# Kernel tuning notes

Measured on AMD Instinct MI355X. Metric: run time of the kernel, lower is better.

Reference implementation:

```python
import jax, jax.numpy as jnp
import numpy as np

N = 50000
E = 800000
IN_C = 512
HID = 256
NUM_CLASS = (10, 25, 16, 350)


def _glorot(key, shape):
    fan_in, fan_out = shape[0], shape[1]
    lim = float(np.sqrt(6.0 / (fan_in + fan_out)))
    return jax.random.uniform(key, shape, jnp.float32, -lim, lim)


def setup_inputs() -> dict:
    key = jax.random.key(0)
    ks = jax.random.split(key, 16)
    x = jax.random.normal(ks[0], (N, IN_C), jnp.float32)
    edge_index = jax.random.randint(ks[1], (2, E), 0, N, jnp.int32)
    inp = {"x": x, "edge_index": edge_index}
    # gc1
    inp["W1"] = _glorot(ks[2], (IN_C, HID)); inp["b1"] = jnp.zeros((HID,), jnp.float32)
    # four GCNConv heads
    names = ["type", "school", "time", "author"]
    for i, (nm, nc) in enumerate(zip(names, NUM_CLASS)):
        inp[f"Wg_{nm}"] = _glorot(ks[3 + i], (HID, nc))
        inp[f"bg_{nm}"] = jnp.zeros((nc,), jnp.float32)
        inp[f"Wc_{nm}"] = _glorot(ks[7 + i], (nc, nc))
        inp[f"bc_{nm}"] = jnp.zeros((nc,), jnp.float32)
    return inp


def gcn_conv(x, W, b, src, dst, n):
    # GCNConv: out = D^{-1/2} (A + I) D^{-1/2} (x W) + b, symmetric norm.
    xw = x @ W  # [N, out]
    ones = jnp.ones((src.shape[0],), xw.dtype)
    deg = jax.ops.segment_sum(ones, dst, num_segments=n) + 1.0  # +1 from self-loop
    dinv = jax.lax.rsqrt(deg)
    norm = dinv[src] * dinv[dst]  # [E]
    agg = jax.ops.segment_sum(xw[src] * norm[:, None], dst, num_segments=n)
    # self-loop contribution: norm_ii = dinv_i^2
    return agg + xw * (dinv * dinv)[:, None] + b


def reference(x, edge_index, W1, b1,
              Wg_type, bg_type, Wc_type, bc_type,
              Wg_school, bg_school, Wc_school, bc_school,
              Wg_time, bg_time, Wc_time, bc_time,
              Wg_author, bg_author, Wc_author, bc_author):
    src, dst = edge_index[0], edge_index[1]
    n = x.shape[0]
    h = jax.nn.relu(gcn_conv(x, W1, b1, src, dst, n))  # dropout is identity in eval

    def head(Wg, bg, Wc, bc):
        g = gcn_conv(h, Wg, bg, src, dst, n)
        return jax.nn.softmax(g @ Wc + bc, axis=-1)

    out_type = head(Wg_type, bg_type, Wc_type, bc_type)
    out_school = head(Wg_school, bg_school, Wc_school, bc_school)
    out_time = head(Wg_time, bg_time, Wc_time, bc_time)
    out_author = head(Wg_author, bg_author, Wc_author, bc_author)
    return (out_type, out_school, out_time, out_author)
```

## Files before the change

kernel.cpp:

```cpp
#include <hip/hip_runtime.h>
#include <hip/hip_bf16.h>
#include <cstdint>
#include <cstddef>
#include <math.h>

#define NN 50000
#define NE 800000
#define INC 512
#define HIDC 256
#define NBLK ((NN + 255) / 256)

typedef __attribute__((ext_vector_type(8))) short s8v;
typedef __attribute__((ext_vector_type(4))) float f4v;
typedef unsigned int u32;

__device__ __forceinline__ float b2f(unsigned short u) {
    return __uint_as_float(((unsigned)u) << 16);
}
__device__ __forceinline__ unsigned short f2b(float f) {
    __hip_bfloat16 h = __float2bfloat16(f);
    return *reinterpret_cast<unsigned short*>(&h);
}
__device__ __forceinline__ void gload16(const void* g, void* l) {
    __builtin_amdgcn_global_load_lds(
        (const __attribute__((address_space(1))) u32*)g,
        (__attribute__((address_space(3))) u32*)l, 16, 0, 0);
}

__global__ void k_deg_count(const int* __restrict__ dst, int* __restrict__ cnt, int e) {
    int i = blockIdx.x * 256 + threadIdx.x;
    if (i < e) atomicAdd(&cnt[dst[i]], 1);
}
__global__ void k_scan1(const int* __restrict__ cnt, int* __restrict__ excl,
                        int* __restrict__ bsum, float* __restrict__ dinv, int n) {
    __shared__ int s[256];
    int i = blockIdx.x * 256 + threadIdx.x;
    int v = (i < n) ? cnt[i] : 0;
    if (i < n) dinv[i] = rsqrtf((float)v + 1.0f);
    s[threadIdx.x] = v;
    __syncthreads();
    for (int off = 1; off < 256; off <<= 1) {
        int t = (threadIdx.x >= off) ? s[threadIdx.x - off] : 0;
        __syncthreads();
        s[threadIdx.x] += t;
        __syncthreads();
    }
    if (i < n) excl[i] = s[threadIdx.x] - v;
    if (threadIdx.x == 255) bsum[blockIdx.x] = s[255];
}
__global__ void k_scan2(int* __restrict__ bsum, int* __restrict__ bsumx, int nb) {
    __shared__ int s[256];
    int t = threadIdx.x;
    int v = (t < nb) ? bsum[t] : 0;
    s[t] = v;
    __syncthreads();
    for (int off = 1; off < 256; off <<= 1) {
        int tt = (t >= off) ? s[t - off] : 0;
        __syncthreads();
        s[t] += tt;
        __syncthreads();
    }
    if (t < nb) bsumx[t] = s[t] - v;
}
__global__ void k_scan3(int* __restrict__ rowptr, const int* __restrict__ bsumx, int n, int e) {
    int i = blockIdx.x * 256 + threadIdx.x;
    if (i < n) rowptr[i] += bsumx[blockIdx.x];
    if (i == 0) rowptr[n] = e;
}
__global__ void k_fill(const int* __restrict__ src, const int* __restrict__ dst,
                       const int* __restrict__ rowptr, int* __restrict__ cursor,
                       int* __restrict__ col, int e) {
    int i = blockIdx.x * 256 + threadIdx.x;
    if (i >= e) return;
    int d = dst[i];
    int pos = rowptr[d] + atomicAdd(&cursor[d], 1);
    col[pos] = src[i];
}

__global__ void k_tr2(const float* __restrict__ Wg3, const float* __restrict__ Wc3,
                      float* __restrict__ Wg3t, float* __restrict__ Wc3t) {
    int t = blockIdx.x * 256 + threadIdx.x;
    if (t < 256 * 350) { int k = t / 350, i = t - k * 350; Wg3t[i * 256 + k] = Wg3[t]; }
    if (t < 350 * 350) { int i = t / 350, j = t - i * 350; Wc3t[j * 350 + i] = Wc3[t]; }
}

__global__ void k_prep(const float* __restrict__ W1,
                       const float* __restrict__ Wg0, const float* __restrict__ Wc0,
                       const float* __restrict__ bg0, const float* __restrict__ bc0,
                       const float* __restrict__ Wg1, const float* __restrict__ Wc1,
                       const float* __restrict__ bg1, const float* __restrict__ bc1,
                       const float* __restrict__ Wg2, const float* __restrict__ Wc2,
                       const float* __restrict__ bg2, const float* __restrict__ bc2,
                       const float* __restrict__ Wg3, const float* __restrict__ Wc3,
                       const float* __restrict__ bg3, const float* __restrict__ bc3,
                       const float* __restrict__ Wg3t, const float* __restrict__ Wc3t,
                       unsigned short* __restrict__ W1t_sw, unsigned short* __restrict__ Wft_sw,
                       float* __restrict__ bfv)
{
    __shared__ float Wcj[352];
    int b = blockIdx.x, tid = threadIdx.x;
    if (b < 512) {
        int t = b * 256 + tid;
        int c = t >> 9, k = t & 511;
        int chs = ((k >> 3) & 7) ^ (c & 7);
        W1t_sw[(size_t)(k >> 6) * 16384 + c * 64 + chs * 8 + (k & 7)] = f2b(W1[(size_t)k * 256 + c]);
    } else if (b < 960) {
        int j = b - 512, k = tid;
        float s = 0.f;
        if (j < 350) {
            for (int i = tid; i < 350; i += 256) Wcj[i] = Wc3t[(size_t)j * 350 + i];
            __syncthreads();
            for (int i = 0; i < 350; ++i) s += Wg3t[i * 256 + k] * Wcj[i];
        } else if (j >= 352 && j < 362) {
            int jj = j - 352; for (int i = 0; i < 10; ++i) s += Wg0[k * 10 + i] * Wc0[i * 10 + jj];
        } else if (j >= 362 && j < 387) {
            int jj = j - 362; for (int i = 0; i < 25; ++i) s += Wg1[k * 25 + i] * Wc1[i * 25 + jj];
        } else if (j >= 387 && j < 403) {
            int jj = j - 387; for (int i = 0; i < 16; ++i) s += Wg2[k * 16 + i] * Wc2[i * 16 + jj];
        }
        int chs = ((k >> 3) & 7) ^ (j & 7);
        Wft_sw[(size_t)(k >> 6) * 28672 + j * 64 + chs * 8 + (k & 7)] = f2b(s);
    } else {
        int j = (b - 960) * 256 + tid;
        if (j >= 448) return;
        float s = 0.f;
        if (j < 350)                  { s = bc3[j]; for (int i = 0; i < 350; ++i) s += bg3[i] * Wc3[(size_t)i * 350 + j]; }
        else if (j >= 352 && j < 362) { int jj = j - 352; s = bc0[jj]; for (int i = 0; i < 10; ++i) s += bg0[i] * Wc0[i * 10 + jj]; }
        else if (j >= 362 && j < 387) { int jj = j - 362; s = bc1[jj]; for (int i = 0; i < 25; ++i) s += bg1[i] * Wc1[i * 25 + jj]; }
        else if (j >= 387 && j < 403) { int jj = j - 387; s = bc2[jj]; for (int i = 0; i < 16; ++i) s += bg2[i] * Wc2[i * 16 + jj]; }
        bfv[j] = s;
    }
}

__global__ __launch_bounds__(256, 4) void gemm1_conv(
    const float* __restrict__ X, const unsigned short* __restrict__ Bsw,
    unsigned short* __restrict__ C, int M)
{
    __shared__ s8v lds[512 + 2048];
    const int t = threadIdx.x;
    const int lane = t & 63, wv = t >> 6;
    const int wvM = wv >> 1, wvN = wv & 1;
    const int l15 = lane & 15, lq = lane >> 4;
    const int row0 = blockIdx.x * 64;

    const int arow = t >> 2;
    int gr = row0 + arow; if (gr >= M) gr = M - 1;
    const float* asrc = X + (size_t)gr * INC + (t & 3) * 16;
    const int ach0 = (t & 3) * 2;
    s8v* aw0 = &lds[arow * 8 + (ach0 ^ (arow & 7))];
    s8v* aw1 = &lds[arow * 8 + ((ach0 + 1) ^ (arow & 7))];

    f4v acc[2][8] = {};
    for (int kb = 0; kb < 8; ++kb) {
        float4 f0 = *(const float4*)(asrc + kb * 64);
        float4 f1 = *(const float4*)(asrc + kb * 64 + 4);
        float4 f2 = *(const float4*)(asrc + kb * 64 + 8);
        float4 f3 = *(const float4*)(asrc + kb * 64 + 12);
        s8v o0, o1;
        o0[0]=(short)f2b(f0.x); o0[1]=(short)f2b(f0.y); o0[2]=(short)f2b(f0.z); o0[3]=(short)f2b(f0.w);
        o0[4]=(short)f2b(f1.x); o0[5]=(short)f2b(f1.y); o0[6]=(short)f2b(f1.z); o0[7]=(short)f2b(f1.w);
        o1[0]=(short)f2b(f2.x); o1[1]=(short)f2b(f2.y); o1[2]=(short)f2b(f2.z); o1[3]=(short)f2b(f2.w);
        o1[4]=(short)f2b(f3.x); o1[5]=(short)f2b(f3.y); o1[6]=(short)f2b(f3.z); o1[7]=(short)f2b(f3.w);
        *aw0 = o0; *aw1 = o1;
#pragma unroll
        for (int sB = 0; sB < 8; ++sB) {
            int ci = (wv * 8 + sB) * 64 + lane;
            gload16(Bsw + ((size_t)kb * 2048 + ci) * 8, (void*)&lds[512 + (wv * 8 + sB) * 64]);
        }
        __syncthreads();
#pragma unroll
        for (int kk = 0; kk < 2; ++kk) {
            const int chr = (kk * 4 + lq) ^ (l15 & 7);
            s8v a0 = lds[(wvM * 32 + l15) * 8 + chr];
            s8v a1 = lds[(wvM * 32 + 16 + l15) * 8 + chr];
#pragma unroll
            for (int cf = 0; cf < 8; ++cf) {
                s8v bf = lds[512 + (wvN * 128 + cf * 16 + l15) * 8 + chr];
                acc[0][cf] = __builtin_amdgcn_mfma_f32_16x16x32_bf16(a0, bf, acc[0][cf], 0, 0, 0);
                acc[1][cf] = __builtin_amdgcn_mfma_f32_16x16x32_bf16(a1, bf, acc[1][cf], 0, 0, 0);
            }
        }
        __syncthreads();
    }
#pragma unroll
    for (int rf = 0; rf < 2; ++rf)
#pragma unroll
    for (int r = 0; r < 4; ++r) {
        int row = row0 + wvM * 32 + rf * 16 + lq * 4 + r;
        if (row >= M) continue;
#pragma unroll
        for (int cf = 0; cf < 8; ++cf)
            C[(size_t)row * HIDC + wvN * 128 + cf * 16 + l15] = f2b(acc[rf][cf][r]);
    }
}

template <bool RELU, bool BIAS, bool SWZ>
__global__ __launch_bounds__(256) void k_gather2(
    const unsigned short* __restrict__ feat, const int* __restrict__ rowptr,
    const int* __restrict__ col, const float* __restrict__ dinv,
    const float* __restrict__ bias, unsigned short* __restrict__ out, int n)
{
    int unit = (blockIdx.x * 256 + threadIdx.x) >> 5;
    int l32 = threadIdx.x & 31;
    if (unit >= n) return;
    float di = dinv[unit];
    int p0 = rowptr[unit], p1 = rowptr[unit + 1];
    int deg = p1 - p0;
    int myc = 0; float mydj = 0.f;
    if (l32 < deg) { myc = col[p0 + l32]; mydj = dinv[myc]; }
    float acc[8] = {};
    int dmin = deg < 32 ? deg : 32;
    int base = threadIdx.x & 32;
#pragma unroll 2
    for (int q = 0; q < dmin; ++q) {
        int j = __shfl(myc, base + q);
        float dj = __shfl(mydj, base + q);
        s8v v = *(const s8v*)(feat + (size_t)j * HIDC + l32 * 8);
#pragma unroll
        for (int c = 0; c < 8; ++c) acc[c] += dj * b2f((unsigned short)v[c]);
    }
    for (int p = p0 + 32; p < p1; ++p) {
        int j = col[p];
        float dj = dinv[j];
        s8v v = *(const s8v*)(feat + (size_t)j * HIDC + l32 * 8);
#pragma unroll
        for (int c = 0; c < 8; ++c) acc[c] += dj * b2f((unsigned short)v[c]);
    }
    s8v sv = *(const s8v*)(feat + (size_t)unit * HIDC + l32 * 8);
    float dd = di * di;
    s8v o;
#pragma unroll
    for (int c = 0; c < 8; ++c) {
        float r = di * acc[c] + dd * b2f((unsigned short)sv[c]);
        if (BIAS) r += bias[l32 * 8 + c];
        if (RELU) r = fmaxf(r, 0.f);
        o[c] = (short)f2b(r);
    }
    int outch = SWZ ? ((l32 & 24) | ((l32 & 7) ^ (unit & 7))) : l32;
    *(s8v*)(out + (size_t)unit * HIDC + outch * 8) = o;
}

__global__ __launch_bounds__(512, 4) void gemm2_heads(
    const unsigned short* __restrict__ Asw, const unsigned short* __restrict__ Bsw,
    const float* __restrict__ bfv,
    float* __restrict__ o0, float* __restrict__ o1,
    float* __restrict__ o2, float* __restrict__ o3, int M)
{
    __shared__ s8v lds[512 + 3584];
    const int t = threadIdx.x;
    const int lane = t & 63, wv = t >> 6;
    const int wvM = wv >> 2, wvN = wv & 3;
    const int l15 = lane & 15, lq = lane >> 4;
    const int row0 = blockIdx.x * 64;

    f4v acc[2][7] = {};
    for (int kb = 0; kb < 4; ++kb) {
        {
            int ci = wv * 64 + lane;
            int arow = ci >> 3, ch = ci & 7;
            int grow = row0 + arow; if (grow >= M) grow = M - 1;
            gload16(Asw + (size_t)grow * HIDC + (kb * 8 + ch) * 8, (void*)&lds[wv * 64]);
        }
#pragma unroll
        for (int sB = 0; sB < 7; ++sB) {
            int ci = (wv * 7 + sB) * 64 + lane;
            gload16(Bsw + ((size_t)kb * 3584 + ci) * 8, (void*)&lds[512 + (wv * 7 + sB) * 64]);
        }
        __syncthreads();
#pragma unroll
        for (int kk = 0; kk < 2; ++kk) {
            const int chr = (kk * 4 + lq) ^ (l15 & 7);
            s8v a0 = lds[(wvM * 32 + l15) * 8 + chr];
            s8v a1 = lds[(wvM * 32 + 16 + l15) * 8 + chr];
#pragma unroll
            for (int cf = 0; cf < 7; ++cf) {
                s8v bf = lds[512 + (wvN * 112 + cf * 16 + l15) * 8 + chr];
                acc[0][cf] = __builtin_amdgcn_mfma_f32_16x16x32_bf16(a0, bf, acc[0][cf], 0, 0, 0);
                acc[1][cf] = __builtin_amdgcn_mfma_f32_16x16x32_bf16(a1, bf, acc[1][cf], 0, 0, 0);
            }
        }
        __syncthreads();
    }
    float* smx = (float*)lds;
#pragma unroll
    for (int cf = 0; cf < 7; ++cf) {
        float bb = bfv[wvN * 112 + cf * 16 + l15];
#pragma unroll
        for (int rf = 0; rf < 2; ++rf)
#pragma unroll
        for (int r = 0; r < 4; ++r) acc[rf][cf][r] += bb;
    }
#pragma unroll
    for (int rf = 0; rf < 2; ++rf)
#pragma unroll
    for (int r = 0; r < 4; ++r) {
        float ma = -1e30f, m1 = -1e30f, m2 = -1e30f, m3 = -1e30f;
#pragma unroll
        for (int cf = 0; cf < 7; ++cf) {
            int colc = wvN * 112 + cf * 16 + l15;
            float v = acc[rf][cf][r];
            if (colc < 350) ma = fmaxf(ma, v);
            else if (colc >= 352 && colc < 362) m1 = fmaxf(m1, v);
            else if (colc >= 362 && colc < 387) m2 = fmaxf(m2, v);
            else if (colc >= 387 && colc < 403) m3 = fmaxf(m3, v);
        }
#pragma unroll
        for (int o = 8; o; o >>= 1) {
            ma = fmaxf(ma, __shfl_xor(ma, o));
            m1 = fmaxf(m1, __shfl_xor(m1, o));
            m2 = fmaxf(m2, __shfl_xor(m2, o));
            m3 = fmaxf(m3, __shfl_xor(m3, o));
        }
        int rowl = wvM * 32 + rf * 16 + lq * 4 + r;
        if (l15 == 0) {
            smx[rowl * 4 + wvN] = ma;
            if (wvN == 3) {
                smx[512 + rowl * 3 + 0] = m1;
                smx[512 + rowl * 3 + 1] = m2;
                smx[512 + rowl * 3 + 2] = m3;
            }
        }
    }
    __syncthreads();
#pragma unroll
    for (int rf = 0; rf < 2; ++rf)
#pragma unroll
    for (int r = 0; r < 4; ++r) {
        int rowl = wvM * 32 + rf * 16 + lq * 4 + r;
        float am = fmaxf(fmaxf(smx[rowl * 4 + 0], smx[rowl * 4 + 1]),
                         fmaxf(smx[rowl * 4 + 2], smx[rowl * 4 + 3]));
        float m1 = 0.f, m2 = 0.f, m3 = 0.f;
        if (wvN == 3) {
            m1 = smx[512 + rowl * 3 + 0];
            m2 = smx[512 + rowl * 3 + 1];
            m3 = smx[512 + rowl * 3 + 2];
        }
        float sa = 0.f, s1 = 0.f, s2 = 0.f, s3 = 0.f;
#pragma unroll
        for (int cf = 0; cf < 7; ++cf) {
            int colc = wvN * 112 + cf * 16 + l15;
            float v = acc[rf][cf][r];
            float e = 0.f;
            if (colc < 350)                     { e = __expf(v - am); sa += e; }
            else if (colc >= 352 && colc < 362) { e = __expf(v - m1); s1 += e; }
            else if (colc >= 362 && colc < 387) { e = __expf(v - m2); s2 += e; }
            else if (colc >= 387 && colc < 403) { e = __expf(v - m3); s3 += e; }
            acc[rf][cf][r] = e;
        }
#pragma unroll
        for (int o = 8; o; o >>= 1) {
            sa += __shfl_xor(sa, o); s1 += __shfl_xor(s1, o);
            s2 += __shfl_xor(s2, o); s3 += __shfl_xor(s3, o);
        }
        if (l15 == 0) {
            smx[256 + rowl * 4 + wvN] = sa;
            if (wvN == 3) {
                smx[704 + rowl * 3 + 0] = s1;
                smx[704 + rowl * 3 + 1] = s2;
                smx[704 + rowl * 3 + 2] = s3;
            }
        }
    }
    __syncthreads();
#pragma unroll
    for (int rf = 0; rf < 2; ++rf)
#pragma unroll
    for (int r = 0; r < 4; ++r) {
        int rowl = wvM * 32 + rf * 16 + lq * 4 + r;
        int row = row0 + rowl;
        if (row >= M) continue;
        float ia = 1.f / (smx[256 + rowl * 4 + 0] + smx[256 + rowl * 4 + 1] +
                          smx[256 + rowl * 4 + 2] + smx[256 + rowl * 4 + 3]);
        float i1 = 0.f, i2 = 0.f, i3 = 0.f;
        if (wvN == 3) {
            i1 = 1.f / smx[704 + rowl * 3 + 0];
            i2 = 1.f / smx[704 + rowl * 3 + 1];
            i3 = 1.f / smx[704 + rowl * 3 + 2];
        }
#pragma unroll
        for (int cf = 0; cf < 7; ++cf) {
            int colc = wvN * 112 + cf * 16 + l15;
            float e = acc[rf][cf][r];
            if (colc < 350)                     o3[(size_t)row * 350 + colc]        = e * ia;
            else if (colc >= 352 && colc < 362) o0[(size_t)row * 10 + (colc - 352)] = e * i1;
            else if (colc >= 362 && colc < 387) o1[(size_t)row * 25 + (colc - 362)] = e * i2;
            else if (colc >= 387 && colc < 403) o2[(size_t)row * 16 + (colc - 387)] = e * i3;
        }
    }
}

extern "C" void kernel_launch(void* const* d_in, const int* in_sizes, int n_in,
                              void* d_out, int out_size, void* d_ws, size_t ws_size,
                              hipStream_t stream)
{
    const float* x   = (const float*)d_in[0];
    const int*   ei  = (const int*)d_in[1];
    const float* W1  = (const float*)d_in[2];
    const float* b1  = (const float*)d_in[3];
    const float* Wg0 = (const float*)d_in[4];
    const float* bg0 = (const float*)d_in[5];
    const float* Wc0 = (const float*)d_in[6];
    const float* bc0 = (const float*)d_in[7];
    const float* Wg1 = (const float*)d_in[8];
    const float* bg1 = (const float*)d_in[9];
    const float* Wc1 = (const float*)d_in[10];
    const float* bc1 = (const float*)d_in[11];
    const float* Wg2 = (const float*)d_in[12];
    const float* bg2 = (const float*)d_in[13];
    const float* Wc2 = (const float*)d_in[14];
    const float* bc2 = (const float*)d_in[15];
    const float* Wg3 = (const float*)d_in[16];
    const float* bg3 = (const float*)d_in[17];
    const float* Wc3 = (const float*)d_in[18];
    const float* bc3 = (const float*)d_in[19];
    const int* srcI = ei;
    const int* dstI = ei + NE;

    char* ws = (char*)d_ws;
    size_t off = 0;
    auto alloc = [&](size_t bytes) { void* p = ws + off; off += (bytes + 255) & ~(size_t)255; return p; };
    float* dinv   = (float*)alloc(50176 * 4);
    int*   rowptr = (int*)  alloc(50432 * 4);
    int*   cnt    = (int*)  alloc(2 * 50176 * 4);
    int*   cursor = cnt + 50176;
    int*   bsum   = (int*)  alloc(1024);
    int*   bsumx  = (int*)  alloc(1024);
    int*   col    = (int*)  alloc((size_t)NE * 4);
    unsigned short* W1t_sw = (unsigned short*)alloc(256 * 512 * 2);
    unsigned short* Wft_sw = (unsigned short*)alloc(448 * 256 * 2);
    float* bfv   = (float*)alloc(448 * 4);
    float* Wg3t  = (float*)alloc(350 * 256 * 4);
    float* Wc3t  = (float*)alloc(350 * 350 * 4);
    unsigned short* xwb = (unsigned short*)alloc((size_t)NN * HIDC * 2);
    unsigned short* hb  = (unsigned short*)alloc((size_t)NN * HIDC * 2);
    unsigned short* ahb = xwb;

    float* out0 = (float*)d_out;
    float* out1 = out0 + (size_t)NN * 10;
    float* out2 = out1 + (size_t)NN * 25;
    float* out3 = out2 + (size_t)NN * 16;

    hipMemsetAsync(cnt, 0, 2 * 50176 * 4, stream);
    k_deg_count<<<(NE + 255) / 256, 256, 0, stream>>>(dstI, cnt, NE);
    k_scan1<<<NBLK, 256, 0, stream>>>(cnt, rowptr, bsum, dinv, NN);
    k_scan2<<<1, 256, 0, stream>>>(bsum, bsumx, NBLK);
    k_scan3<<<NBLK, 256, 0, stream>>>(rowptr, bsumx, NN, NE);
    k_fill<<<(NE + 255) / 256, 256, 0, stream>>>(srcI, dstI, rowptr, cursor, col, NE);

    k_tr2<<<(350 * 350 + 255) / 256, 256, 0, stream>>>(Wg3, Wc3, Wg3t, Wc3t);
    k_prep<<<962, 256, 0, stream>>>(W1,
                                    Wg0, Wc0, bg0, bc0, Wg1, Wc1, bg1, bc1,
                                    Wg2, Wc2, bg2, bc2, Wg3, Wc3, bg3, bc3,
                                    Wg3t, Wc3t, W1t_sw, Wft_sw, bfv);

    gemm1_conv<<<(NN + 63) / 64, 256, 0, stream>>>(x, W1t_sw, xwb, NN);
    k_gather2<true, true, false><<<(NN + 7) / 8, 256, 0, stream>>>(xwb, rowptr, col, dinv, b1, hb, NN);
    k_gather2<false, false, true><<<(NN + 7) / 8, 256, 0, stream>>>(hb, rowptr, col, dinv, nullptr, ahb, NN);
    gemm2_heads<<<(NN + 63) / 64, 512, 0, stream>>>(ahb, Wft_sw, bfv, out0, out1, out2, out3, NN);
}
```

Measured before the change: 341.7 us.

## Double-buffer LDS staging in both GEMMs and repack head weights into k32 panels

Both GEMM kernels now use double-buffered LDS, so the next K-slice's global loads are issued before the MFMAs on the current slice, with explicit vmcnt/lgkmcnt waits and raw barriers in place of __syncthreads. gemm2_heads changes from K-blocks of 64 with XOR-swizzled chunks to K-blocks of 32 in a packed panel layout. That drops the swizzle in the second gather's output and in the prep kernel. gemm1 raises its LDS footprint and lowers the launch-bounds occupancy hint from 4 to 2, trading occupancy for overlap; the unswizzled 32-wide LDS reads may hit bank conflicts.

```diff
diff --git a/kernel.cpp b/kernel.cpp
--- a/kernel.cpp
+++ b/kernel.cpp
@@ -13,6 +13,10 @@
 typedef __attribute__((ext_vector_type(8))) short s8v;
 typedef __attribute__((ext_vector_type(4))) float f4v;
 typedef unsigned int u32;
+
+#define VMC(n)  asm volatile("s_waitcnt vmcnt(" #n ")" ::: "memory")
+#define LGKM0   asm volatile("s_waitcnt lgkmcnt(0)" ::: "memory")
+#define BAR()   do { __builtin_amdgcn_s_barrier(); asm volatile("" ::: "memory"); } while (0)
 
 __device__ __forceinline__ float b2f(unsigned short u) {
     return __uint_as_float(((unsigned)u) << 16);
@@ -94,7 +98,7 @@
                        const float* __restrict__ Wg3, const float* __restrict__ Wc3,
                        const float* __restrict__ bg3, const float* __restrict__ bc3,
                        const float* __restrict__ Wg3t, const float* __restrict__ Wc3t,
-                       unsigned short* __restrict__ W1t_sw, unsigned short* __restrict__ Wft_sw,
+                       unsigned short* __restrict__ W1t_sw, unsigned short* __restrict__ Wftp,
                        float* __restrict__ bfv)
 {
     __shared__ float Wcj[352];
@@ -118,8 +122,7 @@
         } else if (j >= 387 && j < 403) {
             int jj = j - 387; for (int i = 0; i < 16; ++i) s += Wg2[k * 16 + i] * Wc2[i * 16 + jj];
         }
-        int chs = ((k >> 3) & 7) ^ (j & 7);
-        Wft_sw[(size_t)(k >> 6) * 28672 + j * 64 + chs * 8 + (k & 7)] = f2b(s);
+        Wftp[((size_t)(k >> 5) * 448 + j) * 32 + (k & 31)] = f2b(s);
     } else {
         int j = (b - 960) * 256 + tid;
         if (j >= 448) return;
@@ -132,55 +135,68 @@
     }
 }
 
-__global__ __launch_bounds__(256, 4) void gemm1_conv(
+__global__ __launch_bounds__(256, 2) void gemm1_conv(
     const float* __restrict__ X, const unsigned short* __restrict__ Bsw,
     unsigned short* __restrict__ C, int M)
 {
-    __shared__ s8v lds[512 + 2048];
+    __shared__ s8v lds[5120];
     const int t = threadIdx.x;
     const int lane = t & 63, wv = t >> 6;
     const int wvM = wv >> 1, wvN = wv & 1;
     const int l15 = lane & 15, lq = lane >> 4;
     const int row0 = blockIdx.x * 64;
 
-    const int arow = t >> 2;
+    const int arow = t >> 2, q = t & 3;
     int gr = row0 + arow; if (gr >= M) gr = M - 1;
-    const float* asrc = X + (size_t)gr * INC + (t & 3) * 16;
-    const int ach0 = (t & 3) * 2;
-    s8v* aw0 = &lds[arow * 8 + (ach0 ^ (arow & 7))];
-    s8v* aw1 = &lds[arow * 8 + ((ach0 + 1) ^ (arow & 7))];
+    const float* asrc = X + (size_t)gr * INC + q * 16;
+    const int awp0 = arow * 8 + ((q * 2) ^ (arow & 7));
+    const int awp1 = arow * 8 + ((q * 2 + 1) ^ (arow & 7));
+
+    float4 fa0, fa1, fa2, fa3;
+#define STAGE_B1(kbn, buf) do { \
+    const unsigned short* bs_ = Bsw + (size_t)(kbn) * 2048 * 8; \
+    int bb_ = 1024 + (buf) * 2048; \
+    _Pragma("unroll") \
+    for (int sB = 0; sB < 8; ++sB) { \
+        int g_ = (wv * 8 + sB) * 64; \
+        gload16(bs_ + (size_t)(g_ + lane) * 8, (void*)&lds[bb_ + g_]); \
+    } } while (0)
+#define LOAD_A1(kbn) do { \
+    fa0 = *(const float4*)(asrc + (kbn) * 64); \
+    fa1 = *(const float4*)(asrc + (kbn) * 64 + 4); \
+    fa2 = *(const float4*)(asrc + (kbn) * 64 + 8); \
+    fa3 = *(const float4*)(asrc + (kbn) * 64 + 12); } while (0)
 
     f4v acc[2][8] = {};
+    STAGE_B1(0, 0);
+    LOAD_A1(0);
     for (int kb = 0; kb < 8; ++kb) {
-        float4 f0 = *(const float4*)(asrc + kb * 64);
-        float4 f1 = *(const float4*)(asrc + kb * 64 + 4);
-        float4 f2 = *(const float4*)(asrc + kb * 64 + 8);
-        float4 f3 = *(const float4*)(asrc + kb * 64 + 12);
+        const int cur = kb & 1, nxt = cur ^ 1;
+        if (kb < 7) STAGE_B1(kb + 1, nxt);
+        if (kb < 7) { VMC(8); } else { VMC(0); }
         s8v o0, o1;
-        o0[0]=(short)f2b(f0.x); o0[1]=(short)f2b(f0.y); o0[2]=(short)f2b(f0.z); o0[3]=(short)f2b(f0.w);
-        o0[4]=(short)f2b(f1.x); o0[5]=(short)f2b(f1.y); o0[6]=(short)f2b(f1.z); o0[7]=(short)f2b(f1.w);
-        o1[0]=(short)f2b(f2.x); o1[1]=(short)f2b(f2.y); o1[2]=(short)f2b(f2.z); o1[3]=(short)f2b(f2.w);
-        o1[4]=(short)f2b(f3.x); o1[5]=(short)f2b(f3.y); o1[6]=(short)f2b(f3.z); o1[7]=(short)f2b(f3.w);
-        *aw0 = o0; *aw1 = o1;
-#pragma unroll
-        for (int sB = 0; sB < 8; ++sB) {
-            int ci = (wv * 8 + sB) * 64 + lane;
-            gload16(Bsw + ((size_t)kb * 2048 + ci) * 8, (void*)&lds[512 + (wv * 8 + sB) * 64]);
-        }
-        __syncthreads();
+        o0[0]=(short)f2b(fa0.x); o0[1]=(short)f2b(fa0.y); o0[2]=(short)f2b(fa0.z); o0[3]=(short)f2b(fa0.w);
+        o0[4]=(short)f2b(fa1.x); o0[5]=(short)f2b(fa1.y); o0[6]=(short)f2b(fa1.z); o0[7]=(short)f2b(fa1.w);
+        o1[0]=(short)f2b(fa2.x); o1[1]=(short)f2b(fa2.y); o1[2]=(short)f2b(fa2.z); o1[3]=(short)f2b(fa2.w);
+        o1[4]=(short)f2b(fa3.x); o1[5]=(short)f2b(fa3.y); o1[6]=(short)f2b(fa3.z); o1[7]=(short)f2b(fa3.w);
+        lds[cur * 512 + awp0] = o0;
+        lds[cur * 512 + awp1] = o1;
+        if (kb < 7) LOAD_A1(kb + 1);
+        LGKM0; BAR();
+        const int ab = cur * 512, bb = 1024 + cur * 2048;
 #pragma unroll
         for (int kk = 0; kk < 2; ++kk) {
             const int chr = (kk * 4 + lq) ^ (l15 & 7);
-            s8v a0 = lds[(wvM * 32 + l15) * 8 + chr];
-            s8v a1 = lds[(wvM * 32 + 16 + l15) * 8 + chr];
+            s8v a0 = lds[ab + (wvM * 32 + l15) * 8 + chr];
+            s8v a1 = lds[ab + (wvM * 32 + 16 + l15) * 8 + chr];
 #pragma unroll
             for (int cf = 0; cf < 8; ++cf) {
-                s8v bf = lds[512 + (wvN * 128 + cf * 16 + l15) * 8 + chr];
+                s8v bf = lds[bb + (wvN * 128 + cf * 16 + l15) * 8 + chr];
                 acc[0][cf] = __builtin_amdgcn_mfma_f32_16x16x32_bf16(a0, bf, acc[0][cf], 0, 0, 0);
                 acc[1][cf] = __builtin_amdgcn_mfma_f32_16x16x32_bf16(a1, bf, acc[1][cf], 0, 0, 0);
             }
         }
-        __syncthreads();
+        LGKM0; BAR();
     }
 #pragma unroll
     for (int rf = 0; rf < 2; ++rf)
@@ -192,9 +208,11 @@
         for (int cf = 0; cf < 8; ++cf)
             C[(size_t)row * HIDC + wvN * 128 + cf * 16 + l15] = f2b(acc[rf][cf][r]);
     }
-}
-
-template <bool RELU, bool BIAS, bool SWZ>
+#undef STAGE_B1
+#undef LOAD_A1
+}
+
+template <bool RELU, bool BIAS>
 __global__ __launch_bounds__(256) void k_gather2(
     const unsigned short* __restrict__ feat, const int* __restrict__ rowptr,
     const int* __restrict__ col, const float* __restrict__ dinv,
@@ -236,51 +254,62 @@
         if (RELU) r = fmaxf(r, 0.f);
         o[c] = (short)f2b(r);
     }
-    int outch = SWZ ? ((l32 & 24) | ((l32 & 7) ^ (unit & 7))) : l32;
-    *(s8v*)(out + (size_t)unit * HIDC + outch * 8) = o;
+    *(s8v*)(out + (size_t)unit * HIDC + l32 * 8) = o;
 }
 
 __global__ __launch_bounds__(512, 4) void gemm2_heads(
-    const unsigned short* __restrict__ Asw, const unsigned short* __restrict__ Bsw,
+    const unsigned short* __restrict__ Ap, const unsigned short* __restrict__ Bp,
     const float* __restrict__ bfv,
     float* __restrict__ o0, float* __restrict__ o1,
     float* __restrict__ o2, float* __restrict__ o3, int M)
 {
-    __shared__ s8v lds[512 + 3584];
+    __shared__ s8v lds[4096];
     const int t = threadIdx.x;
     const int lane = t & 63, wv = t >> 6;
     const int wvM = wv >> 2, wvN = wv & 3;
     const int l15 = lane & 15, lq = lane >> 4;
     const int row0 = blockIdx.x * 64;
 
+#define STAGE2(kbn, buf) do { \
+    if (wv == 0) { \
+        _Pragma("unroll") \
+        for (int s = 0; s < 4; ++s) { \
+            int ci_ = s * 64 + lane; \
+            int row_ = ci_ >> 2, ch_ = ci_ & 3; \
+            int grow_ = row0 + row_; if (grow_ >= M) grow_ = M - 1; \
+            gload16(Ap + (size_t)grow_ * HIDC + (kbn) * 32 + ch_ * 8, \
+                    (void*)&lds[(buf) * 256 + s * 64]); \
+        } \
+    } else { \
+        _Pragma("unroll") \
+        for (int s = 0; s < 4; ++s) { \
+            int bg_ = (wv - 1) * 4 + s; \
+            int bci_ = bg_ * 64 + lane; \
+            int j_ = bci_ >> 2, ch_ = bci_ & 3; \
+            gload16(Bp + ((size_t)(kbn) * 448 + j_) * 32 + ch_ * 8, \
+                    (void*)&lds[512 + (buf) * 1792 + bg_ * 64]); \
+        } \
+    } } while (0)
+
     f4v acc[2][7] = {};
-    for (int kb = 0; kb < 4; ++kb) {
-        {
-            int ci = wv * 64 + lane;
-            int arow = ci >> 3, ch = ci & 7;
-            int grow = row0 + arow; if (grow >= M) grow = M - 1;
-            gload16(Asw + (size_t)grow * HIDC + (kb * 8 + ch) * 8, (void*)&lds[wv * 64]);
-        }
-#pragma unroll
-        for (int sB = 0; sB < 7; ++sB) {
-            int ci = (wv * 7 + sB) * 64 + lane;
-            gload16(Bsw + ((size_t)kb * 3584 + ci) * 8, (void*)&lds[512 + (wv * 7 + sB) * 64]);
-        }
-        __syncthreads();
-#pragma unroll
-        for (int kk = 0; kk < 2; ++kk) {
-            const int chr = (kk * 4 + lq) ^ (l15 & 7);
-            s8v a0 = lds[(wvM * 32 + l15) * 8 + chr];
-            s8v a1 = lds[(wvM * 32 + 16 + l15) * 8 + chr];
-#pragma unroll
-            for (int cf = 0; cf < 7; ++cf) {
-                s8v bf = lds[512 + (wvN * 112 + cf * 16 + l15) * 8 + chr];
-                acc[0][cf] = __builtin_amdgcn_mfma_f32_16x16x32_bf16(a0, bf, acc[0][cf], 0, 0, 0);
-                acc[1][cf] = __builtin_amdgcn_mfma_f32_16x16x32_bf16(a1, bf, acc[1][cf], 0, 0, 0);
-            }
-        }
-        __syncthreads();
-    }
+    STAGE2(0, 0);
+    for (int kb = 0; kb < 8; ++kb) {
+        const int cur = kb & 1, nxt = cur ^ 1;
+        if (kb < 7) STAGE2(kb + 1, nxt);
+        if (kb < 7) { VMC(4); } else { VMC(0); }
+        LGKM0; BAR();
+        const int ab = cur * 256, bb = 512 + cur * 1792;
+        s8v a0 = lds[ab + (wvM * 32 + l15) * 4 + lq];
+        s8v a1 = lds[ab + (wvM * 32 + 16 + l15) * 4 + lq];
+#pragma unroll
+        for (int cf = 0; cf < 7; ++cf) {
+            s8v bf = lds[bb + (wvN * 112 + cf * 16 + l15) * 4 + lq];
+            acc[0][cf] = __builtin_amdgcn_mfma_f32_16x16x32_bf16(a0, bf, acc[0][cf], 0, 0, 0);
+            acc[1][cf] = __builtin_amdgcn_mfma_f32_16x16x32_bf16(a1, bf, acc[1][cf], 0, 0, 0);
+        }
+        LGKM0; BAR();
+    }
+#undef STAGE2
     float* smx = (float*)lds;
 #pragma unroll
     for (int cf = 0; cf < 7; ++cf) {
@@ -427,7 +456,7 @@
     int*   bsumx  = (int*)  alloc(1024);
     int*   col    = (int*)  alloc((size_t)NE * 4);
     unsigned short* W1t_sw = (unsigned short*)alloc(256 * 512 * 2);
-    unsigned short* Wft_sw = (unsigned short*)alloc(448 * 256 * 2);
+    unsigned short* Wftp   = (unsigned short*)alloc(448 * 256 * 2);
     float* bfv   = (float*)alloc(448 * 4);
     float* Wg3t  = (float*)alloc(350 * 256 * 4);
     float* Wc3t  = (float*)alloc(350 * 350 * 4);
@@ -451,10 +480,10 @@
     k_prep<<<962, 256, 0, stream>>>(W1,
                                     Wg0, Wc0, bg0, bc0, Wg1, Wc1, bg1, bc1,
                                     Wg2, Wc2, bg2, bc2, Wg3, Wc3, bg3, bc3,
-                                    Wg3t, Wc3t, W1t_sw, Wft_sw, bfv);
+                                    Wg3t, Wc3t, W1t_sw, Wftp, bfv);
 
     gemm1_conv<<<(NN + 63) / 64, 256, 0, stream>>>(x, W1t_sw, xwb, NN);
-    k_gather2<true, true, false><<<(NN + 7) / 8, 256, 0, stream>>>(xwb, rowptr, col, dinv, b1, hb, NN);
-    k_gather2<false, false, true><<<(NN + 7) / 8, 256, 0, stream>>>(hb, rowptr, col, dinv, nullptr, ahb, NN);
-    gemm2_heads<<<(NN + 63) / 64, 512, 0, stream>>>(ahb, Wft_sw, bfv, out0, out1, out2, out3, NN);
-}
+    k_gather2<true, true><<<(NN + 7) / 8, 256, 0, stream>>>(xwb, rowptr, col, dinv, b1, hb, NN);
+    k_gather2<false, false><<<(NN + 7) / 8, 256, 0, stream>>>(hb, rowptr, col, dinv, nullptr, ahb, NN);
+    gemm2_heads<<<(NN + 63) / 64, 512, 0, stream>>>(ahb, Wftp, bfv, out0, out1, out2, out3, NN);
+}
```

Result: slower. 360.2 us (+5.4%).

## Load GEMM operands directly from global into registers, dropping LDS staging

Applied to the files above, without the earlier changes.

Both GEMM kernels now load MFMA A and B fragments straight from global memory into registers instead of staging tiles through swizzled shared memory with barriers. The weight prep writes plain transposed layouts, and the gather kernel no longer writes a swizzled output. This removes the LDS traffic and the __syncthreads barriers. In exchange, waves duplicate global loads of the same A rows and B columns, and access is less coalesced, leaning on cache hits.

```diff
diff --git a/kernel.cpp b/kernel.cpp
--- a/kernel.cpp
+++ b/kernel.cpp
@@ -12,7 +12,6 @@
 
 typedef __attribute__((ext_vector_type(8))) short s8v;
 typedef __attribute__((ext_vector_type(4))) float f4v;
-typedef unsigned int u32;
 
 __device__ __forceinline__ float b2f(unsigned short u) {
     return __uint_as_float(((unsigned)u) << 16);
@@ -20,11 +19,6 @@
 __device__ __forceinline__ unsigned short f2b(float f) {
     __hip_bfloat16 h = __float2bfloat16(f);
     return *reinterpret_cast<unsigned short*>(&h);
-}
-__device__ __forceinline__ void gload16(const void* g, void* l) {
-    __builtin_amdgcn_global_load_lds(
-        (const __attribute__((address_space(1))) u32*)g,
-        (__attribute__((address_space(3))) u32*)l, 16, 0, 0);
 }
 
 __global__ void k_deg_count(const int* __restrict__ dst, int* __restrict__ cnt, int e) {
@@ -94,7 +88,7 @@
                        const float* __restrict__ Wg3, const float* __restrict__ Wc3,
                        const float* __restrict__ bg3, const float* __restrict__ bc3,
                        const float* __restrict__ Wg3t, const float* __restrict__ Wc3t,
-                       unsigned short* __restrict__ W1t_sw, unsigned short* __restrict__ Wft_sw,
+                       unsigned short* __restrict__ W1t, unsigned short* __restrict__ Wft,
                        float* __restrict__ bfv)
 {
     __shared__ float Wcj[352];
@@ -102,8 +96,7 @@
     if (b < 512) {
         int t = b * 256 + tid;
         int c = t >> 9, k = t & 511;
-        int chs = ((k >> 3) & 7) ^ (c & 7);
-        W1t_sw[(size_t)(k >> 6) * 16384 + c * 64 + chs * 8 + (k & 7)] = f2b(W1[(size_t)k * 256 + c]);
+        W1t[(size_t)c * 512 + k] = f2b(W1[(size_t)k * 256 + c]);
     } else if (b < 960) {
         int j = b - 512, k = tid;
         float s = 0.f;
@@ -118,8 +111,7 @@
         } else if (j >= 387 && j < 403) {
             int jj = j - 387; for (int i = 0; i < 16; ++i) s += Wg2[k * 16 + i] * Wc2[i * 16 + jj];
         }
-        int chs = ((k >> 3) & 7) ^ (j & 7);
-        Wft_sw[(size_t)(k >> 6) * 28672 + j * 64 + chs * 8 + (k & 7)] = f2b(s);
+        Wft[(size_t)j * 256 + k] = f2b(s);
     } else {
         int j = (b - 960) * 256 + tid;
         if (j >= 448) return;
@@ -132,55 +124,42 @@
     }
 }
 
-__global__ __launch_bounds__(256, 4) void gemm1_conv(
-    const float* __restrict__ X, const unsigned short* __restrict__ Bsw,
+__global__ __launch_bounds__(256) void gemm1_conv(
+    const float* __restrict__ X, const unsigned short* __restrict__ Bt,
     unsigned short* __restrict__ C, int M)
 {
-    __shared__ s8v lds[512 + 2048];
     const int t = threadIdx.x;
     const int lane = t & 63, wv = t >> 6;
     const int wvM = wv >> 1, wvN = wv & 1;
     const int l15 = lane & 15, lq = lane >> 4;
     const int row0 = blockIdx.x * 64;
 
-    const int arow = t >> 2;
-    int gr = row0 + arow; if (gr >= M) gr = M - 1;
-    const float* asrc = X + (size_t)gr * INC + (t & 3) * 16;
-    const int ach0 = (t & 3) * 2;
-    s8v* aw0 = &lds[arow * 8 + (ach0 ^ (arow & 7))];
-    s8v* aw1 = &lds[arow * 8 + ((ach0 + 1) ^ (arow & 7))];
+    int r0 = row0 + wvM * 32 + l15;      if (r0 >= M) r0 = M - 1;
+    int r1 = row0 + wvM * 32 + 16 + l15; if (r1 >= M) r1 = M - 1;
+    const float* a0p = X + (size_t)r0 * INC + lq * 8;
+    const float* a1p = X + (size_t)r1 * INC + lq * 8;
+    const unsigned short* bp = Bt + (size_t)(wvN * 128 + l15) * INC + lq * 8;
 
     f4v acc[2][8] = {};
-    for (int kb = 0; kb < 8; ++kb) {
-        float4 f0 = *(const float4*)(asrc + kb * 64);
-        float4 f1 = *(const float4*)(asrc + kb * 64 + 4);
-        float4 f2 = *(const float4*)(asrc + kb * 64 + 8);
-        float4 f3 = *(const float4*)(asrc + kb * 64 + 12);
-        s8v o0, o1;
-        o0[0]=(short)f2b(f0.x); o0[1]=(short)f2b(f0.y); o0[2]=(short)f2b(f0.z); o0[3]=(short)f2b(f0.w);
-        o0[4]=(short)f2b(f1.x); o0[5]=(short)f2b(f1.y); o0[6]=(short)f2b(f1.z); o0[7]=(short)f2b(f1.w);
-        o1[0]=(short)f2b(f2.x); o1[1]=(short)f2b(f2.y); o1[2]=(short)f2b(f2.z); o1[3]=(short)f2b(f2.w);
-        o1[4]=(short)f2b(f3.x); o1[5]=(short)f2b(f3.y); o1[6]=(short)f2b(f3.z); o1[7]=(short)f2b(f3.w);
-        *aw0 = o0; *aw1 = o1;
-#pragma unroll
-        for (int sB = 0; sB < 8; ++sB) {
-            int ci = (wv * 8 + sB) * 64 + lane;
-            gload16(Bsw + ((size_t)kb * 2048 + ci) * 8, (void*)&lds[512 + (wv * 8 + sB) * 64]);
-        }
-        __syncthreads();
-#pragma unroll
-        for (int kk = 0; kk < 2; ++kk) {
-            const int chr = (kk * 4 + lq) ^ (l15 & 7);
-            s8v a0 = lds[(wvM * 32 + l15) * 8 + chr];
-            s8v a1 = lds[(wvM * 32 + 16 + l15) * 8 + chr];
-#pragma unroll
-            for (int cf = 0; cf < 8; ++cf) {
-                s8v bf = lds[512 + (wvN * 128 + cf * 16 + l15) * 8 + chr];
-                acc[0][cf] = __builtin_amdgcn_mfma_f32_16x16x32_bf16(a0, bf, acc[0][cf], 0, 0, 0);
-                acc[1][cf] = __builtin_amdgcn_mfma_f32_16x16x32_bf16(a1, bf, acc[1][cf], 0, 0, 0);
-            }
-        }
-        __syncthreads();
+    for (int kb = 0; kb < 16; ++kb) {
+        float4 fa0 = *(const float4*)(a0p + kb * 32);
+        float4 fa1 = *(const float4*)(a0p + kb * 32 + 4);
+        float4 fb0 = *(const float4*)(a1p + kb * 32);
+        float4 fb1 = *(const float4*)(a1p + kb * 32 + 4);
+        s8v bfr[8];
+#pragma unroll
+        for (int cf = 0; cf < 8; ++cf)
+            bfr[cf] = *(const s8v*)(bp + (size_t)cf * 16 * INC + kb * 32);
+        s8v a0, a1;
+        a0[0]=(short)f2b(fa0.x); a0[1]=(short)f2b(fa0.y); a0[2]=(short)f2b(fa0.z); a0[3]=(short)f2b(fa0.w);
+        a0[4]=(short)f2b(fa1.x); a0[5]=(short)f2b(fa1.y); a0[6]=(short)f2b(fa1.z); a0[7]=(short)f2b(fa1.w);
+        a1[0]=(short)f2b(fb0.x); a1[1]=(short)f2b(fb0.y); a1[2]=(short)f2b(fb0.z); a1[3]=(short)f2b(fb0.w);
+        a1[4]=(short)f2b(fb1.x); a1[5]=(short)f2b(fb1.y); a1[6]=(short)f2b(fb1.z); a1[7]=(short)f2b(fb1.w);
+#pragma unroll
+        for (int cf = 0; cf < 8; ++cf) {
+            acc[0][cf] = __builtin_amdgcn_mfma_f32_16x16x32_bf16(a0, bfr[cf], acc[0][cf], 0, 0, 0);
+            acc[1][cf] = __builtin_amdgcn_mfma_f32_16x16x32_bf16(a1, bfr[cf], acc[1][cf], 0, 0, 0);
+        }
     }
 #pragma unroll
     for (int rf = 0; rf < 2; ++rf)
@@ -194,7 +173,7 @@
     }
 }
 
-template <bool RELU, bool BIAS, bool SWZ>
+template <bool RELU, bool BIAS>
 __global__ __launch_bounds__(256) void k_gather2(
     const unsigned short* __restrict__ feat, const int* __restrict__ rowptr,
     const int* __restrict__ col, const float* __restrict__ dinv,
@@ -236,52 +215,42 @@
         if (RELU) r = fmaxf(r, 0.f);
         o[c] = (short)f2b(r);
     }
-    int outch = SWZ ? ((l32 & 24) | ((l32 & 7) ^ (unit & 7))) : l32;
-    *(s8v*)(out + (size_t)unit * HIDC + outch * 8) = o;
-}
-
-__global__ __launch_bounds__(512, 4) void gemm2_heads(
-    const unsigned short* __restrict__ Asw, const unsigned short* __restrict__ Bsw,
+    *(s8v*)(out + (size_t)unit * HIDC + l32 * 8) = o;
+}
+
+__global__ __launch_bounds__(512) void gemm2_heads(
+    const unsigned short* __restrict__ A, const unsigned short* __restrict__ B,
     const float* __restrict__ bfv,
     float* __restrict__ o0, float* __restrict__ o1,
     float* __restrict__ o2, float* __restrict__ o3, int M)
 {
-    __shared__ s8v lds[512 + 3584];
+    __shared__ float smx[896];
     const int t = threadIdx.x;
     const int lane = t & 63, wv = t >> 6;
     const int wvM = wv >> 2, wvN = wv & 3;
     const int l15 = lane & 15, lq = lane >> 4;
     const int row0 = blockIdx.x * 64;
 
+    int r0 = row0 + wvM * 32 + l15;      if (r0 >= M) r0 = M - 1;
+    int r1 = row0 + wvM * 32 + 16 + l15; if (r1 >= M) r1 = M - 1;
+    const unsigned short* a0p = A + (size_t)r0 * HIDC + lq * 8;
+    const unsigned short* a1p = A + (size_t)r1 * HIDC + lq * 8;
+    const unsigned short* bp  = B + (size_t)(wvN * 112 + l15) * HIDC + lq * 8;
+
     f4v acc[2][7] = {};
-    for (int kb = 0; kb < 4; ++kb) {
-        {
-            int ci = wv * 64 + lane;
-            int arow = ci >> 3, ch = ci & 7;
-            int grow = row0 + arow; if (grow >= M) grow = M - 1;
-            gload16(Asw + (size_t)grow * HIDC + (kb * 8 + ch) * 8, (void*)&lds[wv * 64]);
-        }
-#pragma unroll
-        for (int sB = 0; sB < 7; ++sB) {
-            int ci = (wv * 7 + sB) * 64 + lane;
-            gload16(Bsw + ((size_t)kb * 3584 + ci) * 8, (void*)&lds[512 + (wv * 7 + sB) * 64]);
-        }
-        __syncthreads();
-#pragma unroll
-        for (int kk = 0; kk < 2; ++kk) {
-            const int chr = (kk * 4 + lq) ^ (l15 & 7);
-            s8v a0 = lds[(wvM * 32 + l15) * 8 + chr];
-            s8v a1 = lds[(wvM * 32 + 16 + l15) * 8 + chr];
-#pragma unroll
-            for (int cf = 0; cf < 7; ++cf) {
-                s8v bf = lds[512 + (wvN * 112 + cf * 16 + l15) * 8 + chr];
-                acc[0][cf] = __builtin_amdgcn_mfma_f32_16x16x32_bf16(a0, bf, acc[0][cf], 0, 0, 0);
-                acc[1][cf] = __builtin_amdgcn_mfma_f32_16x16x32_bf16(a1, bf, acc[1][cf], 0, 0, 0);
-            }
-        }
-        __syncthreads();
-    }
-    float* smx = (float*)lds;
+    for (int kb = 0; kb < 8; ++kb) {
+        s8v a0 = *(const s8v*)(a0p + kb * 32);
+        s8v a1 = *(const s8v*)(a1p + kb * 32);
+        s8v bfr[7];
+#pragma unroll
+        for (int cf = 0; cf < 7; ++cf)
+            bfr[cf] = *(const s8v*)(bp + (size_t)cf * 16 * HIDC + kb * 32);
+#pragma unroll
+        for (int cf = 0; cf < 7; ++cf) {
+            acc[0][cf] = __builtin_amdgcn_mfma_f32_16x16x32_bf16(a0, bfr[cf], acc[0][cf], 0, 0, 0);
+            acc[1][cf] = __builtin_amdgcn_mfma_f32_16x16x32_bf16(a1, bfr[cf], acc[1][cf], 0, 0, 0);
+        }
+    }
 #pragma unroll
     for (int cf = 0; cf < 7; ++cf) {
         float bb = bfv[wvN * 112 + cf * 16 + l15];
@@ -426,8 +395,8 @@
     int*   bsum   = (int*)  alloc(1024);
     int*   bsumx  = (int*)  alloc(1024);
     int*   col    = (int*)  alloc((size_t)NE * 4);
-    unsigned short* W1t_sw = (unsigned short*)alloc(256 * 512 * 2);
-    unsigned short* Wft_sw = (unsigned short*)alloc(448 * 256 * 2);
+    unsigned short* W1t = (unsigned short*)alloc(256 * 512 * 2);
+    unsigned short* Wft = (unsigned short*)alloc(448 * 256 * 2);
     float* bfv   = (float*)alloc(448 * 4);
     float* Wg3t  = (float*)alloc(350 * 256 * 4);
     float* Wc3t  = (float*)alloc(350 * 350 * 4);
@@ -451,10 +420,10 @@
     k_prep<<<962, 256, 0, stream>>>(W1,
                                     Wg0, Wc0, bg0, bc0, Wg1, Wc1, bg1, bc1,
                                     Wg2, Wc2, bg2, bc2, Wg3, Wc3, bg3, bc3,
-                                    Wg3t, Wc3t, W1t_sw, Wft_sw, bfv);
-
-    gemm1_conv<<<(NN + 63) / 64, 256, 0, stream>>>(x, W1t_sw, xwb, NN);
-    k_gather2<true, true, false><<<(NN + 7) / 8, 256, 0, stream>>>(xwb, rowptr, col, dinv, b1, hb, NN);
-    k_gather2<false, false, true><<<(NN + 7) / 8, 256, 0, stream>>>(hb, rowptr, col, dinv, nullptr, ahb, NN);
-    gemm2_heads<<<(NN + 63) / 64, 512, 0, stream>>>(ahb, Wft_sw, bfv, out0, out1, out2, out3, NN);
-}
+                                    Wg3t, Wc3t, W1t, Wft, bfv);
+
+    gemm1_conv<<<(NN + 63) / 64, 256, 0, stream>>>(x, W1t, xwb, NN);
+    k_gather2<true, true><<<(NN + 7) / 8, 256, 0, stream>>>(xwb, rowptr, col, dinv, b1, hb, NN);
+    k_gather2<false, false><<<(NN + 7) / 8, 256, 0, stream>>>(hb, rowptr, col, dinv, nullptr, ahb, NN);
+    gemm2_heads<<<(NN + 63) / 64, 512, 0, stream>>>(ahb, Wft, bfv, out0, out1, out2, out3, NN);
+}
```

Measured after the change: 446.6 us. 1.31x slower.
